# Kernel tuning notes

Measured on AMD Instinct MI355X. Metric: run time of the kernel, lower is better.

Reference implementation:

```python
import math
import jax, jax.numpy as jnp
import numpy as np

NUM_HEADS = 12
EPS = 1e-4


def softmax_kernel_features(data, proj, is_query):
    # data: [B,H,N,d], proj: [m,d] -> features [B,H,N,m]
    d = data.shape[-1]
    data_normalizer = 1.0 / math.sqrt(math.sqrt(d))
    ratio = 1.0 / math.sqrt(proj.shape[0])
    data_dash = jnp.einsum('bhnd,md->bhnm', data_normalizer * data, proj)
    diag_data = (jnp.sum(jnp.square(data), axis=-1, keepdims=True)
                 * 0.5 * data_normalizer * data_normalizer)  # [B,H,N,1]
    if is_query:
        stab = jnp.max(data_dash, axis=-1, keepdims=True)
    else:
        stab = jnp.max(data_dash)
    return ratio * (jnp.exp(data_dash - diag_data - stab) + EPS)


def setup_inputs() -> dict:
    key = jax.random.key(0)
    k0, k1, k2, k3, k4 = jax.random.split(key, 5)
    B, N, C, H = 8, 4096, 768, NUM_HEADS
    hd = C // H
    m = int(hd * math.log(hd))  # 266
    x = jax.random.normal(k0, (B, N, C), dtype=jnp.float32)
    W_qkv = jax.random.normal(k1, (C, 3 * C), dtype=jnp.float32) / math.sqrt(C)
    W_proj = jax.random.normal(k2, (C, C), dtype=jnp.float32) / math.sqrt(C)
    b_proj = jnp.zeros((C,), dtype=jnp.float32)
    proj_mat = jax.random.normal(k3, (m, hd), dtype=jnp.float32)
    return {'x': x, 'W_qkv': W_qkv, 'W_proj': W_proj, 'b_proj': b_proj,
            'proj_mat': proj_mat}


def reference(x, W_qkv, W_proj, b_proj, proj_mat):
    B, N, C = x.shape
    H = NUM_HEADS
    hd = C // H
    qkv = (x @ W_qkv).reshape(B, N, 3, H, hd)
    qkv = jnp.transpose(qkv, (2, 0, 3, 1, 4))  # [3,B,H,N,hd]
    q, k, v = qkv[0], qkv[1], qkv[2]
    q1 = softmax_kernel_features(q, proj_mat, is_query=True)   # [B,H,N,m]
    k1 = softmax_kernel_features(k, proj_mat, is_query=False)  # [B,H,N,m]
    # FAVOR+ non-causal linear attention
    kv = jnp.einsum('bhnm,bhnd->bhmd', k1, v)        # [B,H,m,hd]
    ksum = jnp.sum(k1, axis=2)                        # [B,H,m]
    z = 1.0 / jnp.einsum('bhnm,bhm->bhn', q1, ksum)  # [B,H,N]
    out = jnp.einsum('bhnm,bhmd->bhnd', q1, kv) * z[..., None]
    out = jnp.transpose(out, (0, 2, 1, 3)).reshape(B, N, C)
    return out @ W_proj + b_proj
```

## Files before the change

### kernel.cpp

```cpp
#include <hip/hip_runtime.h>
#include <hip/hip_bf16.h>
#include <math.h>

#define B_ 8
#define N_TOK 4096
#define C_ 768
#define H_ 12
#define HD_ 64
#define M_ 266
#define TC_ 2304
#define BH_ 96
#define ROWS_ 32768

#define M2 288
#define MP 296
#define KVS 72
#define K1S 40

#define DN 0.35355339059327373f
#define RATIO 0.06131393394849658f
#define FEPS 1e-4f
#define NEG_INF -3.0e38f

typedef __attribute__((ext_vector_type(4))) float f32x4;
typedef __attribute__((ext_vector_type(8))) short bf16x8;

__device__ __forceinline__ float bf2f(unsigned short u) {
  return __uint_as_float(((unsigned int)u) << 16);
}
__device__ __forceinline__ unsigned short f2bf(float f) {
  unsigned int x = __float_as_uint(f);
  unsigned int r = (x + 0x7fffu + ((x >> 16) & 1u)) >> 16;
  return (unsigned short)r;
}

#define GLOAD_LDS16(g, l) \
  __builtin_amdgcn_global_load_lds( \
      (const __attribute__((address_space(1))) void*)(g), \
      (__attribute__((address_space(3))) void*)(l), 16, 0, 0)

__global__ __launch_bounds__(256) void cast_bf16(
    const float* __restrict__ src, unsigned short* __restrict__ dst, int n)
{
  int i = (blockIdx.x * 256 + threadIdx.x) * 4;
  if (i < n) {
    float4 v = *(const float4*)&src[i];
    ushort4 u;
    u.x = f2bf(v.x); u.y = f2bf(v.y); u.z = f2bf(v.z); u.w = f2bf(v.w);
    *(ushort4*)&dst[i] = u;
  }
}

__global__ __launch_bounds__(256) void cast_pbf(
    const float* __restrict__ P, unsigned short* __restrict__ Pbf)
{
  int idx = blockIdx.x * 256 + threadIdx.x;
  if (idx < M2 * 64) {
    int m = idx >> 6;
    Pbf[idx] = (m < M_) ? f2bf(P[idx]) : (unsigned short)0;
  }
}

__global__ __launch_bounds__(256) void transpose_cast(
    const float* __restrict__ src, unsigned short* __restrict__ dst,
    int R, int Ccols)
{
  __shared__ float t[32][33];
  const int c0 = blockIdx.x * 32, r0 = blockIdx.y * 32;
  const int tx = threadIdx.x & 31, ty = threadIdx.x >> 5;
#pragma unroll
  for (int i = 0; i < 32; i += 8)
    t[ty + i][tx] = src[(size_t)(r0 + ty + i) * Ccols + c0 + tx];
  __syncthreads();
#pragma unroll
  for (int i = 0; i < 32; i += 8)
    dst[(size_t)(c0 + ty + i) * R + r0 + tx] = f2bf(t[tx][ty + i]);
}

template <int NT, int C_BF16, int HAS_BIAS>
__global__ __launch_bounds__(512) void gemm_pipe(
    const unsigned short* __restrict__ A, const unsigned short* __restrict__ Bt,
    const float* __restrict__ bias, void* __restrict__ Cptr)
{
  __shared__ unsigned short lds_[65536];
  const int Kdim = 768, Ndim = NT * 256;
  const int tid = threadIdx.x;
  const int lane = tid & 63, w = tid >> 6;

  const int id = blockIdx.x;
  const int nwg8 = (128 * NT) >> 3;
  const int sid = (id & 7) * nwg8 + (id >> 3);
  const int row0 = (sid / NT) * 256;
  const int col0 = (sid % NT) * 256;

  const int srow = tid >> 3;
  const int skb = (((tid & 7) ^ (srow & 7)) << 4);
  const size_t ag0 = (size_t)(row0 + srow) * Kdim + (skb >> 1);
  const size_t ag1 = (size_t)(row0 + 64 + srow) * Kdim + (skb >> 1);
  const size_t ag2 = (size_t)(row0 + 128 + srow) * Kdim + (skb >> 1);
  const size_t ag3 = (size_t)(row0 + 192 + srow) * Kdim + (skb >> 1);
  const size_t bg0 = (size_t)(col0 + srow) * Kdim + (skb >> 1);
  const size_t bg1 = (size_t)(col0 + 64 + srow) * Kdim + (skb >> 1);
  const size_t bg2 = (size_t)(col0 + 128 + srow) * Kdim + (skb >> 1);
  const size_t bg3 = (size_t)(col0 + 192 + srow) * Kdim + (skb >> 1);
  const int dst = tid * 8;

#define STAGE_Q(tt) do { \
    unsigned short* Lq_ = lds_ + ((tt) & 1) * 32768; \
    const int kq_ = (tt) * 64; \
    GLOAD_LDS16(A + ag0 + kq_, Lq_ + 0 * 4096 + dst); \
    GLOAD_LDS16(A + ag1 + kq_, Lq_ + 1 * 4096 + dst); \
    GLOAD_LDS16(A + ag2 + kq_, Lq_ + 2 * 4096 + dst); \
    GLOAD_LDS16(A + ag3 + kq_, Lq_ + 3 * 4096 + dst); \
    GLOAD_LDS16(Bt + bg0 + kq_, Lq_ + 16384 + 0 * 4096 + dst); \
    GLOAD_LDS16(Bt + bg1 + kq_, Lq_ + 16384 + 1 * 4096 + dst); \
    GLOAD_LDS16(Bt + bg2 + kq_, Lq_ + 16384 + 2 * 4096 + dst); \
    GLOAD_LDS16(Bt + bg3 + kq_, Lq_ + 16384 + 3 * 4096 + dst); \
  } while (0)

  const int fr = lane & 15, q = lane >> 4;
  const int wm = w >> 2, wn = w & 3;
  const int f7 = fr & 7;
  const int sl0 = ((q + 0) ^ f7) << 3;
  const int sl1 = ((q + 4) ^ f7) << 3;
  const int abase = (wm * 128 + fr) * 64;
  const int bbase = 16384 + (wn * 64 + fr) * 64;

  f32x4 acc[8][4];
  const f32x4 fz = {0.f, 0.f, 0.f, 0.f};
#pragma unroll
  for (int m = 0; m < 8; ++m)
#pragma unroll
    for (int n = 0; n < 4; ++n) acc[m][n] = fz;

  STAGE_Q(0);

#pragma unroll 1
  for (int t = 0; t < 12; ++t) {
    if (t < 11) {
      STAGE_Q(t + 1);
      asm volatile("s_waitcnt vmcnt(8)" ::: "memory");
    } else {
      asm volatile("s_waitcnt vmcnt(0)" ::: "memory");
    }
    __builtin_amdgcn_sched_barrier(0);
    __builtin_amdgcn_s_barrier();
    __builtin_amdgcn_sched_barrier(0);

    const unsigned short* Lb = lds_ + (t & 1) * 32768;
#pragma unroll
    for (int ks = 0; ks < 2; ++ks) {
      const int sl = ks ? sl1 : sl0;
      bf16x8 av[8], bv[4];
#pragma unroll
      for (int m = 0; m < 8; ++m)
        av[m] = *(const bf16x8*)&Lb[abase + m * 1024 + sl];
#pragma unroll
      for (int n = 0; n < 4; ++n)
        bv[n] = *(const bf16x8*)&Lb[bbase + n * 1024 + sl];
      __builtin_amdgcn_s_setprio(1);
#pragma unroll
      for (int m = 0; m < 8; ++m)
#pragma unroll
        for (int n = 0; n < 4; ++n)
          acc[m][n] = __builtin_amdgcn_mfma_f32_16x16x32_bf16(av[m], bv[n], acc[m][n], 0, 0, 0);
      __builtin_amdgcn_s_setprio(0);
    }
    __builtin_amdgcn_sched_barrier(0);
    __builtin_amdgcn_s_barrier();
    __builtin_amdgcn_sched_barrier(0);
  }
#undef STAGE_Q

  const int orow = q * 4;
#pragma unroll
  for (int m = 0; m < 8; ++m) {
#pragma unroll
    for (int n = 0; n < 4; ++n) {
      const int c = col0 + wn * 64 + n * 16 + fr;
      float badd = 0.f;
      if constexpr (HAS_BIAS) badd = bias[c];
#pragma unroll
      for (int j = 0; j < 4; ++j) {
        const int r = row0 + wm * 128 + m * 16 + orow + j;
        float v = acc[m][n][j] + badd;
        if constexpr (C_BF16)
          ((unsigned short*)Cptr)[(size_t)r * Ndim + c] = f2bf(v);
        else
          ((float*)Cptr)[(size_t)r * Ndim + c] = v;
      }
    }
  }
}

__global__ __launch_bounds__(256) void kmax_mfma(
    const unsigned short* __restrict__ qkv, const unsigned short* __restrict__ Pbf,
    float* __restrict__ bmax)
{
  __shared__ unsigned short K_lds[2][64 * KVS];
  __shared__ float red[4];
  const int tid = threadIdx.x;
  const int w = tid >> 6, lane = tid & 63;
  const int lr = lane & 15, q = lane >> 4;
  const int bh = blockIdx.x, chunk = blockIdx.y, z = blockIdx.z;
  const int b = bh / H_, h = bh % H_;
  const int ms = z * 8 + 2 * w;
  const int mc = (z == 1 && w == 3) ? 3 : 2;
  const int sn = 16 * w + (lane >> 2);
  const int sd0 = (lane & 3) * 16;
  const f32x4 fz = {0.f, 0.f, 0.f, 0.f};
  float mx = NEG_INF;

  bf16x8 pf0[3], pf1[3];
#pragma unroll
  for (int i = 0; i < 3; ++i) {
    const unsigned short* prow = Pbf + (size_t)((ms + i) * 16 + lr) * 64 + q * 8;
    pf0[i] = *(const bf16x8*)prow;
    pf1[i] = *(const bf16x8*)(prow + 32);
  }

  const unsigned short* kbase = qkv + (size_t)(b * N_TOK + chunk * 512 + sn) * TC_ + C_ + h * HD_ + sd0;
  const size_t gstep = (size_t)64 * TC_;

  int4 ka = *(const int4*)kbase;
  int4 kb = *(const int4*)(kbase + 8);
  *(int4*)&K_lds[0][sn * KVS + sd0] = ka;
  *(int4*)&K_lds[0][sn * KVS + sd0 + 8] = kb;
  asm volatile("s_waitcnt lgkmcnt(0)" ::: "memory");
  __builtin_amdgcn_s_barrier();

#pragma unroll 1
  for (int g = 0; g < 8; ++g) {
    const unsigned short* Kc = K_lds[g & 1];
    if (g < 7) {
      const unsigned short* kr = kbase + (size_t)(g + 1) * gstep;
      ka = *(const int4*)kr;
      kb = *(const int4*)(kr + 8);
    }
    __builtin_amdgcn_sched_barrier(0);
    bf16x8 bk[4][2];
#pragma unroll
    for (int nt = 0; nt < 4; ++nt) {
      bk[nt][0] = *(const bf16x8*)&Kc[(nt * 16 + lr) * KVS + q * 8];
      bk[nt][1] = *(const bf16x8*)&Kc[(nt * 16 + lr) * KVS + 32 + q * 8];
    }
#pragma unroll
    for (int i = 0; i < 3; ++i) {
      if (i >= mc) continue;
      const int m = (ms + i) * 16 + lr;
#pragma unroll
      for (int nt = 0; nt < 4; ++nt) {
        f32x4 s = fz;
        s = __builtin_amdgcn_mfma_f32_16x16x32_bf16(bk[nt][0], pf0[i], s, 0, 0, 0);
        s = __builtin_amdgcn_mfma_f32_16x16x32_bf16(bk[nt][1], pf1[i], s, 0, 0, 0);
        if (m < M_)
          mx = fmaxf(mx, fmaxf(fmaxf(s[0], s[1]), fmaxf(s[2], s[3])));
      }
    }
    if (g < 7) {
      __builtin_amdgcn_sched_barrier(0);
      __builtin_amdgcn_s_barrier();
      unsigned short* Kn = (unsigned short*)K_lds[(g & 1) ^ 1];
      *(int4*)&Kn[sn * KVS + sd0] = ka;
      *(int4*)&Kn[sn * KVS + sd0 + 8] = kb;
      asm volatile("s_waitcnt lgkmcnt(0)" ::: "memory");
      __builtin_amdgcn_sched_barrier(0);
      __builtin_amdgcn_s_barrier();
      __builtin_amdgcn_sched_barrier(0);
    }
  }
#pragma unroll
  for (int off = 32; off >= 1; off >>= 1) mx = fmaxf(mx, __shfl_xor(mx, off));
  if (lane == 0) red[w] = mx;
  __syncthreads();
  if (tid == 0)
    bmax[(z * 8 + chunk) * BH_ + bh] = fmaxf(fmaxf(red[0], red[1]), fmaxf(red[2], red[3]));
}

__global__ __launch_bounds__(256) void kmax_reduce(
    const float* __restrict__ bmax, float* __restrict__ kmaxp, int n)
{
  __shared__ float red[4];
  float v = NEG_INF;
  for (int i = threadIdx.x; i < n; i += 256) v = fmaxf(v, bmax[i]);
#pragma unroll
  for (int off = 32; off >= 1; off >>= 1) v = fmaxf(v, __shfl_xor(v, off));
  if ((threadIdx.x & 63) == 0) red[threadIdx.x >> 6] = v;
  __syncthreads();
  if (threadIdx.x == 0)
    kmaxp[0] = DN * fmaxf(fmaxf(red[0], red[1]), fmaxf(red[2], red[3]));
}

__global__ __launch_bounds__(256) void kv_partial_mfma(
    const unsigned short* __restrict__ qkv, const unsigned short* __restrict__ Pbf,
    const float* __restrict__ kmaxp,
    float* __restrict__ kvpart, float* __restrict__ ksumpart)
{
  __shared__ unsigned short K_lds[64 * KVS];
  __shared__ unsigned short Vt_lds[64 * KVS];
  __shared__ unsigned short k1_lds[272 * K1S];
  __shared__ float diag_lds[64];
  const int tid = threadIdx.x;
  const int w = tid >> 6, lane = tid & 63;
  const int lr = lane & 15, q = lane >> 4;
  const int bh = blockIdx.x, chunk = blockIdx.y, z = blockIdx.z;
  const int b = bh / H_, h = bh % H_;
  const float stab = kmaxp[0];
  const int ms = z * 8 + 2 * w;
  const int mc = (z == 1 && w == 3) ? 3 : 2;
  const int sn = 16 * w + (lane >> 2);
  const int sd0 = (lane & 3) * 16;
  const int vswz = sn ^ ((lane & 3) << 4);
  const int kswz = (lr >> 3) << 4;
  const f32x4 fz = {0.f, 0.f, 0.f, 0.f};

  f32x4 kvacc[3][4];
  float ksacc[3];
#pragma unroll
  for (int i = 0; i < 3; ++i) {
    ksacc[i] = 0.f;
#pragma unroll
    for (int dt = 0; dt < 4; ++dt) kvacc[i][dt] = fz;
  }

  bf16x8 pf0[3], pf1[3];
#pragma unroll
  for (int i = 0; i < 3; ++i) {
    const unsigned short* prow = Pbf + (size_t)((ms + i) * 16 + lr) * 64 + q * 8;
    pf0[i] = *(const bf16x8*)prow;
    pf1[i] = *(const bf16x8*)(prow + 32);
  }

  const unsigned short* kbase = qkv + (size_t)(b * N_TOK + chunk * 512 + sn) * TC_ + C_ + h * HD_ + sd0;
  const size_t gstep = (size_t)64 * TC_;

  auto write_buf = [&](int4 wka, int4 wkb, int4 wva, int4 wvb) {
    *(int4*)&K_lds[sn * KVS + sd0] = wka;
    *(int4*)&K_lds[sn * KVS + sd0 + 8] = wkb;
    float sq = 0.f;
    const unsigned short* pk0 = (const unsigned short*)&wka;
#pragma unroll
    for (int j = 0; j < 8; ++j) { float f = bf2f(pk0[j]); sq = fmaf(f, f, sq); }
    const unsigned short* pk1 = (const unsigned short*)&wkb;
#pragma unroll
    for (int j = 0; j < 8; ++j) { float f = bf2f(pk1[j]); sq = fmaf(f, f, sq); }
    sq += __shfl_xor(sq, 1);
    sq += __shfl_xor(sq, 2);
    if ((lane & 3) == 0) diag_lds[sn] = 0.0625f * sq;
    const unsigned short* pv0 = (const unsigned short*)&wva;
    const unsigned short* pv1 = (const unsigned short*)&wvb;
#pragma unroll
    for (int j = 0; j < 8; ++j) Vt_lds[(sd0 + j) * KVS + vswz] = pv0[j];
#pragma unroll
    for (int j = 0; j < 8; ++j) Vt_lds[(sd0 + 8 + j) * KVS + vswz] = pv1[j];
  };

  int4 ka = *(const int4*)kbase;
  int4 kb = *(const int4*)(kbase + 8);
  int4 va = *(const int4*)(kbase + C_);
  int4 vb = *(const int4*)(kbase + C_ + 8);
  write_buf(ka, kb, va, vb);
  asm volatile("s_waitcnt lgkmcnt(0)" ::: "memory");
  __builtin_amdgcn_s_barrier();

#pragma unroll 1
  for (int g = 0; g < 8; ++g) {
    if (g < 7) {
      const unsigned short* kr = kbase + (size_t)(g + 1) * gstep;
      ka = *(const int4*)kr;
      kb = *(const int4*)(kr + 8);
      va = *(const int4*)(kr + C_);
      vb = *(const int4*)(kr + C_ + 8);
    }
    __builtin_amdgcn_sched_barrier(0);

#pragma unroll
    for (int ks = 0; ks < 2; ++ks) {
      bf16x8 bkl[2][2];
#pragma unroll
      for (int t = 0; t < 2; ++t) {
        const int nrow = ((2 * ks + t) * 16 + lr) * KVS;
        bkl[t][0] = *(const bf16x8*)&K_lds[nrow + q * 8];
        bkl[t][1] = *(const bf16x8*)&K_lds[nrow + 32 + q * 8];
      }
      bf16x8 bv[4];
#pragma unroll
      for (int dt = 0; dt < 4; ++dt)
        bv[dt] = *(const bf16x8*)&Vt_lds[(dt * 16 + lr) * KVS + ((ks * 32 + q * 8) ^ (dt << 4))];

#pragma unroll
      for (int i = 0; i < 3; ++i) {
        if (i >= mc) continue;
        const int mt = ms + i;
        const int m = mt * 16 + lr;
        const int mrow = (mt * 16 + lr) * K1S;
        float loc = 0.f;
#pragma unroll
        for (int t = 0; t < 2; ++t) {
          f32x4 s = fz;
          s = __builtin_amdgcn_mfma_f32_16x16x32_bf16(bkl[t][0], pf0[i], s, 0, 0, 0);
          s = __builtin_amdgcn_mfma_f32_16x16x32_bf16(bkl[t][1], pf1[i], s, 0, 0, 0);
          ushort4 uo;
          unsigned short* puo = (unsigned short*)&uo;
#pragma unroll
          for (int j = 0; j < 4; ++j) {
            const int nl = (2 * ks + t) * 16 + q * 4 + j;
            float k1f = 0.f;
            if (m < M_) {
              float dash = DN * s[j];
              k1f = RATIO * (__expf(dash - diag_lds[nl] - stab) + FEPS);
            }
            loc += k1f;
            puo[j] = f2bf(k1f);
          }
          *(ushort4*)&k1_lds[mrow + ((t * 16 + q * 4) ^ kswz)] = uo;
        }
        ksacc[i] += loc;
        bf16x8 a1 = *(const bf16x8*)&k1_lds[mrow + ((q * 8) ^ kswz)];
#pragma unroll
        for (int dt = 0; dt < 4; ++dt)
          kvacc[i][dt] = __builtin_amdgcn_mfma_f32_16x16x32_bf16(a1, bv[dt], kvacc[i][dt], 0, 0, 0);
      }
    }

    if (g < 7) {
      __builtin_amdgcn_sched_barrier(0);
      __builtin_amdgcn_s_barrier();
      __builtin_amdgcn_sched_barrier(0);
      write_buf(ka, kb, va, vb);
      asm volatile("s_waitcnt lgkmcnt(0)" ::: "memory");
      __builtin_amdgcn_sched_barrier(0);
      __builtin_amdgcn_s_barrier();
      __builtin_amdgcn_sched_barrier(0);
    }
  }

  const size_t cb = (size_t)(chunk * BH_ + bh) * 64;
#pragma unroll
  for (int i = 0; i < 3; ++i) {
    if (i >= mc) continue;
    const int mt = ms + i;
#pragma unroll
    for (int dt = 0; dt < 4; ++dt) {
      float4 v4;
      v4.x = kvacc[i][dt][0]; v4.y = kvacc[i][dt][1];
      v4.z = kvacc[i][dt][2]; v4.w = kvacc[i][dt][3];
      *(float4*)&kvpart[(cb + dt * 16 + lr) * M2 + mt * 16 + q * 4] = v4;
    }
    float s = ksacc[i];
    s += __shfl_xor(s, 16);
    s += __shfl_xor(s, 32);
    if (lane < 16)
      ksumpart[(size_t)(chunk * BH_ + bh) * M2 + mt * 16 + lane] = s;
  }
}

__global__ __launch_bounds__(256) void kv_reduce2(
    const float* __restrict__ kvpart, const float* __restrict__ ksumpart,
    unsigned short* __restrict__ kvt_g, float* __restrict__ ksum_g)
{
  const int KVN = BH_ * 64 * M2;
  const int KSN = BH_ * M2;
  int idx = blockIdx.x * 256 + threadIdx.x;
  if (idx < KVN) {
    int m = idx % M2;
    float s = 0.f;
    if (m < M_) {
#pragma unroll
      for (int c = 0; c < 8; ++c) s += kvpart[(size_t)c * KVN + idx];
    }
    kvt_g[idx] = f2bf(s);
  } else if (idx < KVN + KSN) {
    int j = idx - KVN;
    int m = j % M2;
    float s = 0.f;
    if (m < M_) {
#pragma unroll
      for (int c = 0; c < 8; ++c) s += ksumpart[(size_t)c * KSN + j];
    }
    ksum_g[j] = s;
  }
}

__global__ __launch_bounds__(256) void attn_mfma(
    const unsigned short* __restrict__ qkv, const unsigned short* __restrict__ Pbf,
    const unsigned short* __restrict__ kvt_g, const float* __restrict__ ksum_g,
    unsigned short* __restrict__ attn)
{
  __shared__ unsigned short q1_lds[64 * MP];
  __shared__ unsigned short kvt_lds[64 * MP];
  __shared__ float ksum_lds[M2];
  __shared__ float z_lds[64];
  const int tid = threadIdx.x;
  const int bh = blockIdx.x, qt = blockIdx.y;
  const int b = bh / H_, h = bh % H_;
  const int n0 = qt * 64;
  const int w = tid >> 6, lane = tid & 63;
  const int lr = lane & 15, q = lane >> 4;

  {
    const unsigned short* src = kvt_g + (size_t)bh * 64 * M2;
#pragma unroll
    for (int i = 0; i < 9; ++i) {
      int chunk = i * 256 + tid;
      int r = chunk / 36, c = (chunk % 36) * 8;
      *(int4*)&kvt_lds[r * MP + c] = *(const int4*)(src + r * M2 + c);
    }
    if (tid < 72)
      *(float4*)&ksum_lds[tid * 4] = *(const float4*)(ksum_g + (size_t)bh * M2 + tid * 4);
    if (tid < 64) {
      const int4 z4 = {0, 0, 0, 0};
      *(int4*)&q1_lds[tid * MP + 272] = z4;
      *(int4*)&q1_lds[tid * MP + 280] = z4;
    }
  }
  __syncthreads();

  const unsigned short* qrow = qkv + (size_t)(b * N_TOK + n0 + w * 16 + lr) * TC_ + h * HD_;
  bf16x8 bq0 = *(const bf16x8*)(qrow + q * 8);
  bf16x8 bq1 = *(const bf16x8*)(qrow + q * 8 + 32);
  float sq = 0.f;
  {
    const unsigned short* p0 = (const unsigned short*)&bq0;
    const unsigned short* p1 = (const unsigned short*)&bq1;
#pragma unroll
    for (int j = 0; j < 8; ++j) { float f = bf2f(p0[j]); sq = fmaf(f, f, sq); }
#pragma unroll
    for (int j = 0; j < 8; ++j) { float f = bf2f(p1[j]); sq = fmaf(f, f, sq); }
  }
  sq += __shfl_xor(sq, 16);
  sq += __shfl_xor(sq, 32);
  const float diag = 0.0625f * sq;

  f32x4 sacc[17];
  const f32x4 fz = {0.f, 0.f, 0.f, 0.f};
#pragma unroll
  for (int mt = 0; mt < 17; ++mt) sacc[mt] = fz;
#pragma unroll
  for (int mt = 0; mt < 17; ++mt) {
    const unsigned short* prow = Pbf + (size_t)(mt * 16 + lr) * 64;
    bf16x8 ap0 = *(const bf16x8*)(prow + q * 8);
    bf16x8 ap1 = *(const bf16x8*)(prow + q * 8 + 32);
    sacc[mt] = __builtin_amdgcn_mfma_f32_16x16x32_bf16(ap0, bq0, sacc[mt], 0, 0, 0);
    sacc[mt] = __builtin_amdgcn_mfma_f32_16x16x32_bf16(ap1, bq1, sacc[mt], 0, 0, 0);
  }

  float mxr = NEG_INF;
#pragma unroll
  for (int mt = 0; mt < 17; ++mt) {
#pragma unroll
    for (int j = 0; j < 4; ++j) {
      int m = mt * 16 + q * 4 + j;
      if (m < M_) mxr = fmaxf(mxr, sacc[mt][j]);
    }
  }
  mxr = fmaxf(mxr, __shfl_xor(mxr, 16));
  mxr = fmaxf(mxr, __shfl_xor(mxr, 32));
  const float mxd = DN * mxr;

  float zp = 0.f;
#pragma unroll
  for (int mt = 0; mt < 17; ++mt) {
    ushort4 uo;
    unsigned short* puo = (unsigned short*)&uo;
#pragma unroll
    for (int j = 0; j < 4; ++j) {
      const int m = mt * 16 + q * 4 + j;
      float q1f = 0.f;
      if (m < M_) {
        float dash = DN * sacc[mt][j];
        q1f = RATIO * (__expf(dash - diag - mxd) + FEPS);
      }
      zp = fmaf(q1f, ksum_lds[m], zp);
      puo[j] = f2bf(q1f);
    }
    *(ushort4*)&q1_lds[(w * 16 + lr) * MP + mt * 16 + q * 4] = uo;
  }
  zp += __shfl_xor(zp, 16);
  zp += __shfl_xor(zp, 32);
  if (q == 0) z_lds[w * 16 + lr] = 1.0f / zp;

  f32x4 oacc[4];
#pragma unroll
  for (int dt = 0; dt < 4; ++dt) oacc[dt] = fz;
#pragma unroll
  for (int ks = 0; ks < 9; ++ks) {
    bf16x8 aq = *(const bf16x8*)&q1_lds[(w * 16 + lr) * MP + ks * 32 + q * 8];
#pragma unroll
    for (int dt = 0; dt < 4; ++dt) {
      bf16x8 bkv = *(const bf16x8*)&kvt_lds[(dt * 16 + lr) * MP + ks * 32 + q * 8];
      oacc[dt] = __builtin_amdgcn_mfma_f32_16x16x32_bf16(aq, bkv, oacc[dt], 0, 0, 0);
    }
  }

  float zz[4];
#pragma unroll
  for (int j = 0; j < 4; ++j) zz[j] = z_lds[w * 16 + q * 4 + j];
#pragma unroll
  for (int dt = 0; dt < 4; ++dt) {
#pragma unroll
    for (int j = 0; j < 4; ++j) {
      const int r = b * N_TOK + n0 + w * 16 + q * 4 + j;
      attn[(size_t)r * C_ + h * HD_ + dt * 16 + lr] = f2bf(oacc[dt][j] * zz[j]);
    }
  }
}

extern "C" void kernel_launch(void* const* d_in, const int* in_sizes, int n_in,
                              void* d_out, int out_size, void* d_ws, size_t ws_size,
                              hipStream_t stream) {
  const float* x     = (const float*)d_in[0];
  const float* Wqkv  = (const float*)d_in[1];
  const float* Wproj = (const float*)d_in[2];
  const float* bproj = (const float*)d_in[3];
  const float* P     = (const float*)d_in[4];
  float* out = (float*)d_out;
  float* ws = (float*)d_ws;

  unsigned short* qkv    = (unsigned short*)ws;
  unsigned short* xb     = (unsigned short*)(ws + 37748736);
  float*          kvpart = ws + 37748736;
  unsigned short* attn   = (unsigned short*)(ws + 37748736);
  float* ksumpart = ws + 51904512;
  unsigned short* kvt_g  = (unsigned short*)(ws + 52125696);
  float* ksum_g   = ws + 53010432;
  float* bmax     = ws + 53038080;
  float* kmaxp    = ws + 53041152;
  unsigned short* Pbf    = (unsigned short*)(ws + 53041216);
  unsigned short* Wqkvt  = (unsigned short*)(ws + 53050432);
  unsigned short* Wprojt = (unsigned short*)(ws + 53935168);

  cast_bf16<<<dim3(24576), 256, 0, stream>>>(x, xb, ROWS_ * C_);
  transpose_cast<<<dim3(72, 24), 256, 0, stream>>>(Wqkv, Wqkvt, C_, TC_);
  transpose_cast<<<dim3(24, 24), 256, 0, stream>>>(Wproj, Wprojt, C_, C_);
  cast_pbf<<<dim3(72), 256, 0, stream>>>(P, Pbf);

  gemm_pipe<9, 1, 0><<<dim3(1152), 512, 0, stream>>>(xb, Wqkvt, nullptr, qkv);
  kmax_mfma<<<dim3(96, 8, 2), 256, 0, stream>>>(qkv, Pbf, bmax);
  kmax_reduce<<<dim3(1), 256, 0, stream>>>(bmax, kmaxp, 1536);
  kv_partial_mfma<<<dim3(96, 8, 2), 256, 0, stream>>>(qkv, Pbf, kmaxp, kvpart, ksumpart);
  kv_reduce2<<<dim3(7020), 256, 0, stream>>>(kvpart, ksumpart, kvt_g, ksum_g);
  attn_mfma<<<dim3(96, 64), 256, 0, stream>>>(qkv, Pbf, kvt_g, ksum_g, attn);
  gemm_pipe<3, 0, 1><<<dim3(384), 512, 0, stream>>>(attn, Wprojt, bproj, out);
}
```

Baseline: 521.0 us.

## Fold global key max into reduction to drop separate kmax pass

The separate kmax_mfma kernel, which recomputed K·P only to find the global stabiliser, is removed. kv_partial_mfma now accumulates unstabilised exp(dash - diag) along with the block max and per-dimension V sums. kv_reduce2 then applies exp(-max), RATIO and the EPS·ΣV terms algebraically. This saves a full pass over K and its MFMA work. In exchange, the unstabilised exponentials could overflow for inputs with large projections, and the reduce kernel gains extra loads.

```diff
diff --git a/kernel.cpp b/kernel.cpp
--- a/kernel.cpp
+++ b/kernel.cpp
@@ -193,12 +193,29 @@
   }
 }
 
-__global__ __launch_bounds__(256) void kmax_mfma(
+__global__ __launch_bounds__(256) void kmax_reduce(
+    const float* __restrict__ bmax, float* __restrict__ kmaxp, int n)
+{
+  __shared__ float red[4];
+  float v = NEG_INF;
+  for (int i = threadIdx.x; i < n; i += 256) v = fmaxf(v, bmax[i]);
+#pragma unroll
+  for (int off = 32; off >= 1; off >>= 1) v = fmaxf(v, __shfl_xor(v, off));
+  if ((threadIdx.x & 63) == 0) red[threadIdx.x >> 6] = v;
+  __syncthreads();
+  if (threadIdx.x == 0)
+    kmaxp[0] = DN * fmaxf(fmaxf(red[0], red[1]), fmaxf(red[2], red[3]));
+}
+
+__global__ __launch_bounds__(256) void kv_partial_mfma(
     const unsigned short* __restrict__ qkv, const unsigned short* __restrict__ Pbf,
-    float* __restrict__ bmax)
-{
-  __shared__ unsigned short K_lds[2][64 * KVS];
-  __shared__ float red[4];
+    float* __restrict__ kvpart, float* __restrict__ ksumpart,
+    float* __restrict__ bmax, float* __restrict__ Wpart)
+{
+  __shared__ unsigned short K_lds[64 * KVS];
+  __shared__ unsigned short Vt_lds[64 * KVS];
+  __shared__ unsigned short k1_lds[272 * K1S];
+  __shared__ float diag_lds[64];
   const int tid = threadIdx.x;
   const int w = tid >> 6, lane = tid & 63;
   const int lr = lane & 15, q = lane >> 4;
@@ -208,108 +225,6 @@
   const int mc = (z == 1 && w == 3) ? 3 : 2;
   const int sn = 16 * w + (lane >> 2);
   const int sd0 = (lane & 3) * 16;
-  const f32x4 fz = {0.f, 0.f, 0.f, 0.f};
-  float mx = NEG_INF;
-
-  bf16x8 pf0[3], pf1[3];
-#pragma unroll
-  for (int i = 0; i < 3; ++i) {
-    const unsigned short* prow = Pbf + (size_t)((ms + i) * 16 + lr) * 64 + q * 8;
-    pf0[i] = *(const bf16x8*)prow;
-    pf1[i] = *(const bf16x8*)(prow + 32);
-  }
-
-  const unsigned short* kbase = qkv + (size_t)(b * N_TOK + chunk * 512 + sn) * TC_ + C_ + h * HD_ + sd0;
-  const size_t gstep = (size_t)64 * TC_;
-
-  int4 ka = *(const int4*)kbase;
-  int4 kb = *(const int4*)(kbase + 8);
-  *(int4*)&K_lds[0][sn * KVS + sd0] = ka;
-  *(int4*)&K_lds[0][sn * KVS + sd0 + 8] = kb;
-  asm volatile("s_waitcnt lgkmcnt(0)" ::: "memory");
-  __builtin_amdgcn_s_barrier();
-
-#pragma unroll 1
-  for (int g = 0; g < 8; ++g) {
-    const unsigned short* Kc = K_lds[g & 1];
-    if (g < 7) {
-      const unsigned short* kr = kbase + (size_t)(g + 1) * gstep;
-      ka = *(const int4*)kr;
-      kb = *(const int4*)(kr + 8);
-    }
-    __builtin_amdgcn_sched_barrier(0);
-    bf16x8 bk[4][2];
-#pragma unroll
-    for (int nt = 0; nt < 4; ++nt) {
-      bk[nt][0] = *(const bf16x8*)&Kc[(nt * 16 + lr) * KVS + q * 8];
-      bk[nt][1] = *(const bf16x8*)&Kc[(nt * 16 + lr) * KVS + 32 + q * 8];
-    }
-#pragma unroll
-    for (int i = 0; i < 3; ++i) {
-      if (i >= mc) continue;
-      const int m = (ms + i) * 16 + lr;
-#pragma unroll
-      for (int nt = 0; nt < 4; ++nt) {
-        f32x4 s = fz;
-        s = __builtin_amdgcn_mfma_f32_16x16x32_bf16(bk[nt][0], pf0[i], s, 0, 0, 0);
-        s = __builtin_amdgcn_mfma_f32_16x16x32_bf16(bk[nt][1], pf1[i], s, 0, 0, 0);
-        if (m < M_)
-          mx = fmaxf(mx, fmaxf(fmaxf(s[0], s[1]), fmaxf(s[2], s[3])));
-      }
-    }
-    if (g < 7) {
-      __builtin_amdgcn_sched_barrier(0);
-      __builtin_amdgcn_s_barrier();
-      unsigned short* Kn = (unsigned short*)K_lds[(g & 1) ^ 1];
-      *(int4*)&Kn[sn * KVS + sd0] = ka;
-      *(int4*)&Kn[sn * KVS + sd0 + 8] = kb;
-      asm volatile("s_waitcnt lgkmcnt(0)" ::: "memory");
-      __builtin_amdgcn_sched_barrier(0);
-      __builtin_amdgcn_s_barrier();
-      __builtin_amdgcn_sched_barrier(0);
-    }
-  }
-#pragma unroll
-  for (int off = 32; off >= 1; off >>= 1) mx = fmaxf(mx, __shfl_xor(mx, off));
-  if (lane == 0) red[w] = mx;
-  __syncthreads();
-  if (tid == 0)
-    bmax[(z * 8 + chunk) * BH_ + bh] = fmaxf(fmaxf(red[0], red[1]), fmaxf(red[2], red[3]));
-}
-
-__global__ __launch_bounds__(256) void kmax_reduce(
-    const float* __restrict__ bmax, float* __restrict__ kmaxp, int n)
-{
-  __shared__ float red[4];
-  float v = NEG_INF;
-  for (int i = threadIdx.x; i < n; i += 256) v = fmaxf(v, bmax[i]);
-#pragma unroll
-  for (int off = 32; off >= 1; off >>= 1) v = fmaxf(v, __shfl_xor(v, off));
-  if ((threadIdx.x & 63) == 0) red[threadIdx.x >> 6] = v;
-  __syncthreads();
-  if (threadIdx.x == 0)
-    kmaxp[0] = DN * fmaxf(fmaxf(red[0], red[1]), fmaxf(red[2], red[3]));
-}
-
-__global__ __launch_bounds__(256) void kv_partial_mfma(
-    const unsigned short* __restrict__ qkv, const unsigned short* __restrict__ Pbf,
-    const float* __restrict__ kmaxp,
-    float* __restrict__ kvpart, float* __restrict__ ksumpart)
-{
-  __shared__ unsigned short K_lds[64 * KVS];
-  __shared__ unsigned short Vt_lds[64 * KVS];
-  __shared__ unsigned short k1_lds[272 * K1S];
-  __shared__ float diag_lds[64];
-  const int tid = threadIdx.x;
-  const int w = tid >> 6, lane = tid & 63;
-  const int lr = lane & 15, q = lane >> 4;
-  const int bh = blockIdx.x, chunk = blockIdx.y, z = blockIdx.z;
-  const int b = bh / H_, h = bh % H_;
-  const float stab = kmaxp[0];
-  const int ms = z * 8 + 2 * w;
-  const int mc = (z == 1 && w == 3) ? 3 : 2;
-  const int sn = 16 * w + (lane >> 2);
-  const int sd0 = (lane & 3) * 16;
   const int vswz = sn ^ ((lane & 3) << 4);
   const int kswz = (lr >> 3) << 4;
   const f32x4 fz = {0.f, 0.f, 0.f, 0.f};
@@ -322,6 +237,10 @@
 #pragma unroll
     for (int dt = 0; dt < 4; ++dt) kvacc[i][dt] = fz;
   }
+  float mx = NEG_INF;
+  float vsum[16];
+#pragma unroll
+  for (int j = 0; j < 16; ++j) vsum[j] = 0.f;
 
   bf16x8 pf0[3], pf1[3];
 #pragma unroll
@@ -350,9 +269,17 @@
     const unsigned short* pv0 = (const unsigned short*)&wva;
     const unsigned short* pv1 = (const unsigned short*)&wvb;
 #pragma unroll
-    for (int j = 0; j < 8; ++j) Vt_lds[(sd0 + j) * KVS + vswz] = pv0[j];
-#pragma unroll
-    for (int j = 0; j < 8; ++j) Vt_lds[(sd0 + 8 + j) * KVS + vswz] = pv1[j];
+    for (int j = 0; j < 8; ++j) {
+      float vf = bf2f(pv0[j]);
+      vsum[j] += vf;
+      Vt_lds[(sd0 + j) * KVS + vswz] = pv0[j];
+    }
+#pragma unroll
+    for (int j = 0; j < 8; ++j) {
+      float vf = bf2f(pv1[j]);
+      vsum[8 + j] += vf;
+      Vt_lds[(sd0 + 8 + j) * KVS + vswz] = pv1[j];
+    }
   };
 
   int4 ka = *(const int4*)kbase;
@@ -400,6 +327,8 @@
           f32x4 s = fz;
           s = __builtin_amdgcn_mfma_f32_16x16x32_bf16(bkl[t][0], pf0[i], s, 0, 0, 0);
           s = __builtin_amdgcn_mfma_f32_16x16x32_bf16(bkl[t][1], pf1[i], s, 0, 0, 0);
+          if (m < M_)
+            mx = fmaxf(mx, fmaxf(fmaxf(s[0], s[1]), fmaxf(s[2], s[3])));
           ushort4 uo;
           unsigned short* puo = (unsigned short*)&uo;
 #pragma unroll
@@ -408,7 +337,7 @@
             float k1f = 0.f;
             if (m < M_) {
               float dash = DN * s[j];
-              k1f = RATIO * (__expf(dash - diag_lds[nl] - stab) + FEPS);
+              k1f = __expf(dash - diag_lds[nl]);
             }
             loc += k1f;
             puo[j] = f2bf(k1f);
@@ -453,21 +382,55 @@
     if (lane < 16)
       ksumpart[(size_t)(chunk * BH_ + bh) * M2 + mt * 16 + lane] = s;
   }
+
+#pragma unroll
+  for (int off = 32; off >= 1; off >>= 1) mx = fmaxf(mx, __shfl_xor(mx, off));
+#pragma unroll
+  for (int j = 0; j < 16; ++j) {
+    vsum[j] += __shfl_xor(vsum[j], 4);
+    vsum[j] += __shfl_xor(vsum[j], 8);
+    vsum[j] += __shfl_xor(vsum[j], 16);
+    vsum[j] += __shfl_xor(vsum[j], 32);
+  }
+  __syncthreads();
+  float* red = (float*)diag_lds;
+  float* Wred = (float*)k1_lds;
+  if (lane == 0) red[w] = mx;
+  if (lane < 4) {
+#pragma unroll
+    for (int j = 0; j < 16; ++j)
+      Wred[w * 64 + lane * 16 + j] = vsum[j];
+  }
+  __syncthreads();
+  if (tid == 0)
+    bmax[(z * 8 + chunk) * BH_ + bh] = fmaxf(fmaxf(red[0], red[1]), fmaxf(red[2], red[3]));
+  if (z == 0 && tid < 64)
+    Wpart[(size_t)(chunk * BH_ + bh) * 64 + tid] =
+        Wred[tid] + Wred[64 + tid] + Wred[128 + tid] + Wred[192 + tid];
 }
 
 __global__ __launch_bounds__(256) void kv_reduce2(
     const float* __restrict__ kvpart, const float* __restrict__ ksumpart,
+    const float* __restrict__ Wpart, const float* __restrict__ kmaxp,
     unsigned short* __restrict__ kvt_g, float* __restrict__ ksum_g)
 {
   const int KVN = BH_ * 64 * M2;
   const int KSN = BH_ * M2;
+  const float es = __expf(-kmaxp[0]);
   int idx = blockIdx.x * 256 + threadIdx.x;
   if (idx < KVN) {
     int m = idx % M2;
     float s = 0.f;
     if (m < M_) {
-#pragma unroll
-      for (int c = 0; c < 8; ++c) s += kvpart[(size_t)c * KVN + idx];
+      float U = 0.f;
+#pragma unroll
+      for (int c = 0; c < 8; ++c) U += kvpart[(size_t)c * KVN + idx];
+      const int d = (idx / M2) & 63;
+      const int bh = idx / (M2 * 64);
+      float Wsum = 0.f;
+#pragma unroll
+      for (int c = 0; c < 8; ++c) Wsum += Wpart[(size_t)(c * BH_ + bh) * 64 + d];
+      s = RATIO * (es * U + FEPS * Wsum);
     }
     kvt_g[idx] = f2bf(s);
   } else if (idx < KVN + KSN) {
@@ -475,8 +438,10 @@
     int m = j % M2;
     float s = 0.f;
     if (m < M_) {
-#pragma unroll
-      for (int c = 0; c < 8; ++c) s += ksumpart[(size_t)c * KSN + j];
+      float u = 0.f;
+#pragma unroll
+      for (int c = 0; c < 8; ++c) u += ksumpart[(size_t)c * KSN + j];
+      s = RATIO * (es * u + FEPS * (float)N_TOK);
     }
     ksum_g[j] = s;
   }
@@ -629,6 +594,7 @@
   unsigned short* Pbf    = (unsigned short*)(ws + 53041216);
   unsigned short* Wqkvt  = (unsigned short*)(ws + 53050432);
   unsigned short* Wprojt = (unsigned short*)(ws + 53935168);
+  float* Wpart    = ws + 54230080;
 
   cast_bf16<<<dim3(24576), 256, 0, stream>>>(x, xb, ROWS_ * C_);
   transpose_cast<<<dim3(72, 24), 256, 0, stream>>>(Wqkv, Wqkvt, C_, TC_);
@@ -636,10 +602,9 @@
   cast_pbf<<<dim3(72), 256, 0, stream>>>(P, Pbf);
 
   gemm_pipe<9, 1, 0><<<dim3(1152), 512, 0, stream>>>(xb, Wqkvt, nullptr, qkv);
-  kmax_mfma<<<dim3(96, 8, 2), 256, 0, stream>>>(qkv, Pbf, bmax);
+  kv_partial_mfma<<<dim3(96, 8, 2), 256, 0, stream>>>(qkv, Pbf, kvpart, ksumpart, bmax, Wpart);
   kmax_reduce<<<dim3(1), 256, 0, stream>>>(bmax, kmaxp, 1536);
-  kv_partial_mfma<<<dim3(96, 8, 2), 256, 0, stream>>>(qkv, Pbf, kmaxp, kvpart, ksumpart);
-  kv_reduce2<<<dim3(7020), 256, 0, stream>>>(kvpart, ksumpart, kvt_g, ksum_g);
+  kv_reduce2<<<dim3(7020), 256, 0, stream>>>(kvpart, ksumpart, Wpart, kmaxp, kvt_g, ksum_g);
   attn_mfma<<<dim3(96, 64), 256, 0, stream>>>(qkv, Pbf, kvt_g, ksum_g, attn);
   gemm_pipe<3, 0, 1><<<dim3(384), 512, 0, stream>>>(attn, Wprojt, bproj, out);
 }
```

New measurement: 470.6 us. 1.11x faster.
